# Optimization experiments

Measured on AMD Instinct MI355X. Metric: run time of the kernel, lower is better.

The kernel has to match this reference:

```python
import jax, jax.numpy as jnp
import numpy as np

B, S, H = 32, 1024, 768          # batch, seq_len, bert hidden
E, W, P = 128, 8, 512            # entities/sample, span width, rel pairs/sample
NT, NR = 5, 9                    # entity types, relation types
D1, HEADS1, D2, RD = 128, 2, 64, 32
REL_IN = 2 * D2 + RD + H         # 928


def _layernorm(x, g, b):
    m = x.mean(-1, keepdims=True)
    v = x.var(-1, keepdims=True)
    return (x - m) * jax.lax.rsqrt(v + 1e-5) * g + b


def _gat_dense(x, Wm, a_src, a_dst, bias, concat):
    # Fully-connected entity graph (incl. self-loops, PyG GATConv default).
    Bn, En, _ = x.shape
    Hh, D = a_src.shape
    h = (x @ Wm).reshape(Bn, En, Hh, D)                      # [B,E,h,D]
    s = jnp.einsum('behd,hd->beh', h, a_src)                 # source score
    d = jnp.einsum('behd,hd->beh', h, a_dst)                 # target score
    # edge j->i : e_ij = leaky_relu(s_j + d_i)
    e = jax.nn.leaky_relu(d[:, :, None, :] + s[:, None, :, :], 0.2)  # [B,i,j,h]
    alpha = jax.nn.softmax(e, axis=2)
    o = jnp.einsum('bijh,bjhd->bihd', alpha, h)
    o = o.reshape(Bn, En, Hh * D) if concat else o.mean(axis=2)
    return o + bias


def setup_inputs() -> dict:
    key = jax.random.key(0)
    ks = jax.random.split(key, 20)
    f = lambda k, shape: jax.random.normal(k, shape, jnp.float32) * 0.02
    return dict(
        sequence_output=jax.random.normal(ks[0], (B, S, H), jnp.float32),
        entity_starts=jax.random.randint(ks[1], (B, E), 0, S - W),
        entity_type_ids=jax.random.randint(ks[2], (B, E), 0, NT),
        pair_idx=jax.random.randint(ks[3], (B, P, 2), 0, E),
        rel_type_ids=jax.random.randint(ks[4], (B, P), 0, NR),
        entity_type_emb=f(ks[5], (NT, H)),
        rel_type_emb=f(ks[6], (NR, RD)),
        W1=f(ks[7], (H, HEADS1 * D1)), a_src1=f(ks[8], (HEADS1, D1)),
        a_dst1=f(ks[9], (HEADS1, D1)), b1=jnp.zeros((HEADS1 * D1,), jnp.float32),
        ln1_g=jnp.ones((HEADS1 * D1,), jnp.float32), ln1_b=jnp.zeros((HEADS1 * D1,), jnp.float32),
        W2=f(ks[10], (HEADS1 * D1, D2)), a_src2=f(ks[11], (1, D2)),
        a_dst2=f(ks[12], (1, D2)), b2=jnp.zeros((D2,), jnp.float32),
        ln2_g=jnp.ones((D2,), jnp.float32), ln2_b=jnp.zeros((D2,), jnp.float32),
        Wr1=f(ks[13], (REL_IN, 256)), br1=jnp.zeros((256,), jnp.float32),
        Wr2=f(ks[14], (256, 1)), br2=jnp.zeros((1,), jnp.float32),
    )


def reference(sequence_output, entity_starts, entity_type_ids, pair_idx, rel_type_ids,
              entity_type_emb, rel_type_emb,
              W1, a_src1, a_dst1, b1, ln1_g, ln1_b,
              W2, a_src2, a_dst2, b2, ln2_g, ln2_b,
              Wr1, br1, Wr2, br2):
    bidx = jnp.arange(B)[:, None]
    # --- per-entity attention pooling over span tokens ---
    tok_idx = entity_starts[:, :, None] + jnp.arange(W)            # [B,E,W]
    toks = sequence_output[jnp.arange(B)[:, None, None], tok_idx]  # [B,E,W,H]
    mean = toks.mean(axis=2)                                       # [B,E,H]
    attn = jax.nn.softmax(jnp.einsum('bewh,beh->bew', toks, mean), axis=-1)
    pooled = jnp.einsum('bew,bewh->beh', attn, toks)
    x = pooled + entity_type_emb[entity_type_ids]                  # [B,E,H]
    # --- 2-layer GAT over fully-connected entity graph ---
    x = jax.nn.elu(_layernorm(_gat_dense(x, W1, a_src1, a_dst1, b1, True), ln1_g, ln1_b))
    x = jax.nn.elu(_layernorm(_gat_dense(x, W2, a_src2, a_dst2, b2, False), ln2_g, ln2_b))
    # --- gather-concat relation MLP scoring ---
    cls = sequence_output[:, 0, :]                                 # [B,H]
    x1 = x[bidx, pair_idx[:, :, 0]]                                # [B,P,64]
    x2 = x[bidx, pair_idx[:, :, 1]]
    rel = rel_type_emb[rel_type_ids]                               # [B,P,32]
    pv = jnp.concatenate([x1, x2, rel, jnp.broadcast_to(cls[:, None, :], (B, P, H))], axis=-1)
    scores = (jax.nn.relu(pv @ Wr1 + br1) @ Wr2 + br2)[..., 0]     # [B,P]
    return scores
```

## Files before the change

kernel.cpp:

```cpp
#include <hip/hip_runtime.h>
#include <hip/hip_bf16.h>

#define BB 32
#define SS 1024
#define HHH 768
#define EE 128
#define WW 8
#define PP 512
#define RDD 32

typedef __attribute__((ext_vector_type(8))) short bf16x8;
typedef __attribute__((ext_vector_type(8))) unsigned short us8;
typedef __attribute__((ext_vector_type(4))) unsigned short us4;
typedef __attribute__((ext_vector_type(4))) float f32x4;

__device__ __forceinline__ unsigned short f2bf(float v) {
    __hip_bfloat16 h = __float2bfloat16(v);
    return *(unsigned short*)&h;
}

__global__ __launch_bounds__(256) void pool_prep_kernel(
    const float* __restrict__ seq, const int* __restrict__ starts,
    const int* __restrict__ types, const float* __restrict__ temb,
    unsigned short* __restrict__ xout,
    const float* __restrict__ W1, unsigned short* __restrict__ Wt,
    const float* __restrict__ Wr1, unsigned short* __restrict__ Wtr,
    const float* __restrict__ W2, unsigned short* __restrict__ W2t,
    const float* __restrict__ remb, unsigned short* __restrict__ rembb,
    float* __restrict__ basep) {
    int tid = threadIdx.x;
    __shared__ float sbuf[WW * HHH];
    __shared__ float scred[WW];
    __shared__ float attn_s[WW];

    if (blockIdx.x < BB * EE) {
        int be = blockIdx.x;
        int b = be >> 7;
        int start = starts[be];
        const float4* bp4 = (const float4*)(seq + ((size_t)b * SS + start) * HHH);
        for (int idx = tid; idx < WW * (HHH / 4); idx += 256) {
            int w = idx / (HHH / 4), h4 = idx % (HHH / 4);
            float4 v = bp4[(size_t)w * (HHH / 4) + h4];
            sbuf[w * HHH + h4 * 4 + 0] = v.x; sbuf[w * HHH + h4 * 4 + 1] = v.y;
            sbuf[w * HHH + h4 * 4 + 2] = v.z; sbuf[w * HHH + h4 * 4 + 3] = v.w;
        }
        __syncthreads();

        float sc[WW];
#pragma unroll
        for (int w = 0; w < WW; w++) sc[w] = 0.f;
#pragma unroll
        for (int c = 0; c < 3; c++) {
            int h = tid + 256 * c;
            float s = 0.f;
#pragma unroll
            for (int w = 0; w < WW; w++) s += sbuf[w * HHH + h];
            float m = s * (1.0f / WW);
#pragma unroll
            for (int w = 0; w < WW; w++) sc[w] += sbuf[w * HHH + h] * m;
        }
        if (tid < WW) scred[tid] = 0.f;
        __syncthreads();
        int lane = tid & 63;
#pragma unroll
        for (int w = 0; w < WW; w++) {
            float v = sc[w];
            for (int o = 32; o > 0; o >>= 1) v += __shfl_down(v, o, 64);
            if (lane == 0) atomicAdd(&scred[w], v);
        }
        __syncthreads();
        if (tid == 0) {
            float mx = scred[0];
            for (int w = 1; w < WW; w++) mx = fmaxf(mx, scred[w]);
            float ssum = 0.f;
            float a[WW];
            for (int w = 0; w < WW; w++) { a[w] = __expf(scred[w] - mx); ssum += a[w]; }
            float inv = 1.f / ssum;
            for (int w = 0; w < WW; w++) attn_s[w] = a[w] * inv;
        }
        __syncthreads();

        int t = types[be];
        const float* emb = temb + (size_t)t * HHH;
#pragma unroll
        for (int c = 0; c < 3; c++) {
            int h = tid + 256 * c;
            float p = 0.f;
#pragma unroll
            for (int w = 0; w < WW; w++) p += attn_s[w] * sbuf[w * HHH + h];
            xout[(size_t)be * HHH + h] = f2bf(p + emb[h]);
        }
        return;
    }

    int blk = blockIdx.x - BB * EE;
    if (blk < 48) {
        int k0 = blk * 16;
        for (int i = tid; i < 16 * 256; i += 256)
            sbuf[i] = W1[(size_t)(k0 + (i >> 8)) * 256 + (i & 255)];
        __syncthreads();
        int n = tid;
        us8 v0, v1;
#pragma unroll
        for (int kk = 0; kk < 8; kk++) v0[kk] = f2bf(sbuf[kk * 256 + n]);
#pragma unroll
        for (int kk = 0; kk < 8; kk++) v1[kk] = f2bf(sbuf[(8 + kk) * 256 + n]);
        *(us8*)(Wt + (size_t)n * HHH + k0) = v0;
        *(us8*)(Wt + (size_t)n * HHH + k0 + 8) = v1;
    } else if (blk < 58) {
        int k0 = (blk - 48) * 16;
        for (int i = tid; i < 16 * 256; i += 256)
            sbuf[i] = Wr1[(size_t)(k0 + (i >> 8)) * 256 + (i & 255)];
        __syncthreads();
        int n = tid;
        us8 v0, v1;
#pragma unroll
        for (int kk = 0; kk < 8; kk++) v0[kk] = f2bf(sbuf[kk * 256 + n]);
#pragma unroll
        for (int kk = 0; kk < 8; kk++) v1[kk] = f2bf(sbuf[(8 + kk) * 256 + n]);
        *(us8*)(Wtr + (size_t)n * 160 + k0) = v0;
        *(us8*)(Wtr + (size_t)n * 160 + k0 + 8) = v1;
    } else if (blk < 74) {
        int k0 = (blk - 58) * 16;
        for (int i = tid; i < 16 * 64; i += 256)
            sbuf[(i >> 6) * 64 + (i & 63)] = W2[(size_t)(k0 + (i >> 6)) * 64 + (i & 63)];
        __syncthreads();
        if (tid < 64) {
            int n = tid;
            us8 v0, v1;
#pragma unroll
            for (int kk = 0; kk < 8; kk++) v0[kk] = f2bf(sbuf[kk * 64 + n]);
#pragma unroll
            for (int kk = 0; kk < 8; kk++) v1[kk] = f2bf(sbuf[(8 + kk) * 64 + n]);
            *(us8*)(W2t + (size_t)n * 256 + k0) = v0;
            *(us8*)(W2t + (size_t)n * 256 + k0 + 8) = v1;
        }
    } else if (blk == 74) {
        for (int i = tid; i < 9 * RDD; i += 256) rembb[i] = f2bf(remb[i]);
    } else {
        int pc = blk - 75;
        int kc = pc % 12;
        int b = pc / 12;
        int n = tid;
        if (n < 64) sbuf[4096 + n] = seq[(size_t)b * SS * HHH + kc * 64 + n];
        __syncthreads();
        float acc = 0.f;
        const float* w = Wr1 + (size_t)(160 + kc * 64) * 256 + n;
#pragma unroll 16
        for (int k = 0; k < 64; k++) acc += sbuf[4096 + k] * w[(size_t)k * 256];
        basep[((size_t)kc * 32 + b) * 256 + n] = acc;
    }
}

__global__ __launch_bounds__(256) void gemm1_mfma_kernel(
    const unsigned short* __restrict__ Xb, const unsigned short* __restrict__ Wt,
    const float* __restrict__ asrc1, const float* __restrict__ adst1,
    unsigned short* __restrict__ h1Tg,
    float* __restrict__ ps_s, float* __restrict__ ps_d) {
    const int K = HHH;
    int n0 = blockIdx.x * 64;
    int m0 = blockIdx.y * 64;
    int tid = threadIdx.x;
    int wave = tid >> 6, lane = tid & 63;
    int wm = (wave >> 1) * 32, wn = (wave & 1) * 32;

    __shared__ __align__(16) unsigned short As[64][40];
    __shared__ __align__(16) unsigned short Bs[64][40];
    __shared__ __align__(16) unsigned short T[64][72];
    __shared__ float sdred[64][2][2];

    f32x4 acc[2][2] = {};
    int ar = tid >> 2;
    int ac = (tid & 3) * 8;
    int fr = lane & 15;
    int fk = (lane >> 4) * 8;

    for (int k0 = 0; k0 < K; k0 += 32) {
        us8 av = *(const us8*)(Xb + (size_t)(m0 + ar) * K + k0 + ac);
        us8 bv = *(const us8*)(Wt + (size_t)(n0 + ar) * K + k0 + ac);
        *(us8*)(&As[ar][ac]) = av;
        *(us8*)(&Bs[ar][ac]) = bv;
        __syncthreads();

        bf16x8 a0 = *(const bf16x8*)(&As[wm + fr][fk]);
        bf16x8 a1 = *(const bf16x8*)(&As[wm + 16 + fr][fk]);
        bf16x8 b0 = *(const bf16x8*)(&Bs[wn + fr][fk]);
        bf16x8 b1 = *(const bf16x8*)(&Bs[wn + 16 + fr][fk]);

        acc[0][0] = __builtin_amdgcn_mfma_f32_16x16x32_bf16(a0, b0, acc[0][0], 0, 0, 0);
        acc[0][1] = __builtin_amdgcn_mfma_f32_16x16x32_bf16(a0, b1, acc[0][1], 0, 0, 0);
        acc[1][0] = __builtin_amdgcn_mfma_f32_16x16x32_bf16(a1, b0, acc[1][0], 0, 0, 0);
        acc[1][1] = __builtin_amdgcn_mfma_f32_16x16x32_bf16(a1, b1, acc[1][1], 0, 0, 0);
        __syncthreads();
    }

    int crow = (lane >> 4) * 4;
    int ccol = lane & 15;
    int h = n0 >> 7;
    int nb = (n0 >> 6) & 1;
    int dbase = (n0 & 127) + wn;

    float asv[2], adv[2];
#pragma unroll
    for (int ni = 0; ni < 2; ni++) {
        int d = dbase + ni * 16 + ccol;
        asv[ni] = asrc1[h * 128 + d];
        adv[ni] = adst1[h * 128 + d];
    }

#pragma unroll
    for (int mi = 0; mi < 2; mi++) {
#pragma unroll
        for (int r = 0; r < 4; r++) {
            float sp = 0.f, dp = 0.f;
#pragma unroll
            for (int ni = 0; ni < 2; ni++) {
                float v = acc[mi][ni][r];
                T[wn + ni * 16 + ccol][wm + mi * 16 + crow + r] = f2bf(v);
                sp += v * asv[ni];
                dp += v * adv[ni];
            }
            for (int msk = 1; msk < 16; msk <<= 1) {
                sp += __shfl_xor(sp, msk, 64);
                dp += __shfl_xor(dp, msk, 64);
            }
            if ((lane & 15) == 0) {
                int row = wm + mi * 16 + crow + r;
                sdred[row][wn >> 5][0] = sp;
                sdred[row][wn >> 5][1] = dp;
            }
        }
    }
    __syncthreads();

    int b = m0 >> 7;
    int j0 = m0 & 127;
    if (tid < 64) {
        float spt = sdred[tid][0][0] + sdred[tid][1][0];
        float dpt = sdred[tid][0][1] + sdred[tid][1][1];
        size_t o = (size_t)nb * 8192 + ((size_t)(m0 + tid)) * 2 + h;
        ps_s[o] = spt;
        ps_d[o] = dpt;
    }
    {
        int d_l = tid >> 2, q = tid & 3;
        us8 v0 = *(const us8*)(&T[d_l][q * 16]);
        us8 v1 = *(const us8*)(&T[d_l][q * 16 + 8]);
        size_t go = ((size_t)(b * 2 + h) * 128 + (n0 & 127) + d_l) * 128 + j0 + q * 16;
        *(us8*)(h1Tg + go) = v0;
        *(us8*)(h1Tg + go + 8) = v1;
    }
}

__global__ __launch_bounds__(256) void gat1_gemm2_kernel(
    const unsigned short* __restrict__ h1Tg,
    const float* __restrict__ ps_s, const float* __restrict__ ps_d,
    const float* __restrict__ b1, const float* __restrict__ gamma,
    const float* __restrict__ beta,
    const unsigned short* __restrict__ W2t,
    const float* __restrict__ asrc2, const float* __restrict__ adst2,
    unsigned short* __restrict__ h2Tg, float* __restrict__ s2,
    float* __restrict__ d2) {
    int b = blockIdx.x >> 2;
    int c = blockIdx.x & 3;
    int tid = threadIdx.x;
    int wave = tid >> 6, lane = tid & 63;
    int h = wave >> 1, m = wave & 1;
    int fr = lane & 15;
    int fk = (lane >> 4) * 8;

    __shared__ __align__(16) unsigned short h1T[2][128][136];
    __shared__ float ssh[2][128];
    __shared__ float dsh[2][128];
    __shared__ float lnred[32][2][2];
    __shared__ __align__(16) unsigned short g1s[32][264];
    __shared__ float sdr2[32][2][2];
    __shared__ __align__(16) unsigned short t2[64][40];

    {
        const us8* src = (const us8*)(h1Tg + (size_t)b * 32768);
#pragma unroll
        for (int it = 0; it < 16; it++) {
            int i8 = tid + it * 256;
            int row = i8 >> 4;
            int j8 = i8 & 15;
            *(us8*)(&h1T[row >> 7][row & 127][j8 * 8]) = src[i8];
        }
        int hh = tid >> 7, j = tid & 127;
        size_t o = ((size_t)b * 128 + j) * 2 + hh;
        ssh[hh][j] = ps_s[o] + ps_s[o + 8192];
        dsh[hh][j] = ps_d[o] + ps_d[o + 8192];
    }
    __syncthreads();

    bf16x8 afrag[4];
    {
        float dd = dsh[h][c * 32 + m * 16 + fr];
        float ev[4][8];
        float mx = -1e30f;
#pragma unroll
        for (int ks = 0; ks < 4; ks++)
#pragma unroll
            for (int jj = 0; jj < 8; jj++) {
                float e = dd + ssh[h][ks * 32 + fk + jj];
                e = e >= 0.f ? e : 0.2f * e;
                ev[ks][jj] = e;
                mx = fmaxf(mx, e);
            }
        mx = fmaxf(mx, __shfl_xor(mx, 16, 64));
        mx = fmaxf(mx, __shfl_xor(mx, 32, 64));
        float sm = 0.f;
#pragma unroll
        for (int ks = 0; ks < 4; ks++)
#pragma unroll
            for (int jj = 0; jj < 8; jj++) {
                float e = __expf(ev[ks][jj] - mx);
                ev[ks][jj] = e;
                sm += e;
            }
        sm += __shfl_xor(sm, 16, 64);
        sm += __shfl_xor(sm, 32, 64);
        float inv = 1.f / sm;
#pragma unroll
        for (int ks = 0; ks < 4; ks++) {
            bf16x8 a;
#pragma unroll
            for (int jj = 0; jj < 8; jj++)
                a[jj] = (short)f2bf(ev[ks][jj] * inv);
            afrag[ks] = a;
        }
    }

    f32x4 acc[8] = {};
#pragma unroll
    for (int ks = 0; ks < 4; ks++)
#pragma unroll
        for (int ni = 0; ni < 8; ni++) {
            bf16x8 bv = *(const bf16x8*)(&h1T[h][ni * 16 + fr][ks * 32 + fk]);
            acc[ni] = __builtin_amdgcn_mfma_f32_16x16x32_bf16(
                afrag[ks], bv, acc[ni], 0, 0, 0);
        }

    int crow = (lane >> 4) * 4;
    int ccol = lane & 15;
    float bv_[8], gv[8], bev[8];
#pragma unroll
    for (int ni = 0; ni < 8; ni++) {
        int d = h * 128 + ni * 16 + ccol;
        bv_[ni] = b1[d]; gv[ni] = gamma[d]; bev[ni] = beta[d];
    }
    float vv[4][8];
#pragma unroll
    for (int r = 0; r < 4; r++) {
        float s = 0.f, q = 0.f;
#pragma unroll
        for (int ni = 0; ni < 8; ni++) {
            float v = acc[ni][r] + bv_[ni];
            vv[r][ni] = v;
            s += v;
            q += v * v;
        }
        s += __shfl_xor(s, 1, 64); s += __shfl_xor(s, 2, 64);
        s += __shfl_xor(s, 4, 64); s += __shfl_xor(s, 8, 64);
        q += __shfl_xor(q, 1, 64); q += __shfl_xor(q, 2, 64);
        q += __shfl_xor(q, 4, 64); q += __shfl_xor(q, 8, 64);
        if ((lane & 15) == 0) {
            lnred[m * 16 + crow + r][h][0] = s;
            lnred[m * 16 + crow + r][h][1] = q;
        }
    }
    __syncthreads();
#pragma unroll
    for (int r = 0; r < 4; r++) {
        int row = m * 16 + crow + r;
        float s = lnred[row][0][0] + lnred[row][1][0];
        float q = lnred[row][0][1] + lnred[row][1][1];
        float mean = s * (1.f / 256.f);
        float var = q * (1.f / 256.f) - mean * mean;
        float rs = rsqrtf(var + 1e-5f);
#pragma unroll
        for (int ni = 0; ni < 8; ni++) {
            float y = (vv[r][ni] - mean) * rs * gv[ni] + bev[ni];
            y = y > 0.f ? y : (__expf(y) - 1.f);
            g1s[row][h * 128 + ni * 16 + ccol] = f2bf(y);
        }
    }
    __syncthreads();

    int m2 = wave & 1;
    int nb = wave >> 1;
    f32x4 acc2[2] = {};
#pragma unroll
    for (int kc = 0; kc < 8; kc++) {
        bf16x8 a = *(const bf16x8*)(&g1s[m2 * 16 + fr][kc * 32 + fk]);
#pragma unroll
        for (int ni = 0; ni < 2; ni++) {
            bf16x8 wv = *(const bf16x8*)(W2t + (size_t)(nb * 32 + ni * 16 + fr) * 256 +
                                         kc * 32 + fk);
            acc2[ni] = __builtin_amdgcn_mfma_f32_16x16x32_bf16(a, wv, acc2[ni], 0, 0, 0);
        }
    }
    float as2[2], ad2[2];
#pragma unroll
    for (int ni = 0; ni < 2; ni++) {
        int n = nb * 32 + ni * 16 + ccol;
        as2[ni] = asrc2[n];
        ad2[ni] = adst2[n];
    }
#pragma unroll
    for (int r = 0; r < 4; r++) {
        int rl = m2 * 16 + crow + r;
        float sp = 0.f, dp = 0.f;
#pragma unroll
        for (int ni = 0; ni < 2; ni++) {
            float v = acc2[ni][r];
            t2[nb * 32 + ni * 16 + ccol][rl] = f2bf(v);
            sp += v * as2[ni];
            dp += v * ad2[ni];
        }
        for (int msk = 1; msk < 16; msk <<= 1) {
            sp += __shfl_xor(sp, msk, 64);
            dp += __shfl_xor(dp, msk, 64);
        }
        if ((lane & 15) == 0) {
            sdr2[rl][nb][0] = sp;
            sdr2[rl][nb][1] = dp;
        }
    }
    __syncthreads();
    if (tid < 32) {
        s2[(size_t)b * 128 + c * 32 + tid] = sdr2[tid][0][0] + sdr2[tid][1][0];
        d2[(size_t)b * 128 + c * 32 + tid] = sdr2[tid][0][1] + sdr2[tid][1][1];
    }
    {
        int d = tid >> 2, q = tid & 3;
        us8 v = *(const us8*)(&t2[d][q * 8]);
        *(us8*)(h2Tg + ((size_t)b * 64 + d) * 128 + c * 32 + q * 8) = v;
    }
}

__global__ __launch_bounds__(256) void gat2_fused_kernel(
    const unsigned short* __restrict__ h2Tg, const float* __restrict__ s2,
    const float* __restrict__ d2, const float* __restrict__ b2v,
    const float* __restrict__ gamma, const float* __restrict__ beta,
    unsigned short* __restrict__ x2b) {
    int b = blockIdx.x >> 1;
    int c = blockIdx.x & 1;
    int tid = threadIdx.x;
    int wave = tid >> 6, lane = tid & 63;
    int fr = lane & 15;
    int fk = (lane >> 4) * 8;

    __shared__ __align__(16) unsigned short h2T[64][136];
    __shared__ float ssh[128];
    __shared__ float dsh[128];

    {
        const us8* src = (const us8*)(h2Tg + (size_t)b * 64 * 128);
#pragma unroll
        for (int it = 0; it < 4; it++) {
            int i8 = tid + it * 256;
            int row = i8 >> 4;
            int j8 = i8 & 15;
            *(us8*)(&h2T[row][j8 * 8]) = src[i8];
        }
        if (tid < 128) ssh[tid] = s2[(size_t)b * 128 + tid];
        else dsh[tid - 128] = d2[(size_t)b * 128 + (tid - 128)];
    }
    __syncthreads();

    bf16x8 afrag[4];
    {
        float dd = dsh[c * 64 + wave * 16 + fr];
        float ev[4][8];
        float mx = -1e30f;
#pragma unroll
        for (int ks = 0; ks < 4; ks++)
#pragma unroll
            for (int jj = 0; jj < 8; jj++) {
                float e = dd + ssh[ks * 32 + fk + jj];
                e = e >= 0.f ? e : 0.2f * e;
                ev[ks][jj] = e;
                mx = fmaxf(mx, e);
            }
        mx = fmaxf(mx, __shfl_xor(mx, 16, 64));
        mx = fmaxf(mx, __shfl_xor(mx, 32, 64));
        float sm = 0.f;
#pragma unroll
        for (int ks = 0; ks < 4; ks++)
#pragma unroll
            for (int jj = 0; jj < 8; jj++) {
                float e = __expf(ev[ks][jj] - mx);
                ev[ks][jj] = e;
                sm += e;
            }
        sm += __shfl_xor(sm, 16, 64);
        sm += __shfl_xor(sm, 32, 64);
        float inv = 1.f / sm;
#pragma unroll
        for (int ks = 0; ks < 4; ks++) {
            bf16x8 a;
#pragma unroll
            for (int jj = 0; jj < 8; jj++)
                a[jj] = (short)f2bf(ev[ks][jj] * inv);
            afrag[ks] = a;
        }
    }

    f32x4 acc[4] = {};
#pragma unroll
    for (int ks = 0; ks < 4; ks++)
#pragma unroll
        for (int ni = 0; ni < 4; ni++) {
            bf16x8 bv = *(const bf16x8*)(&h2T[ni * 16 + fr][ks * 32 + fk]);
            acc[ni] = __builtin_amdgcn_mfma_f32_16x16x32_bf16(
                afrag[ks], bv, acc[ni], 0, 0, 0);
        }

    int crow = (lane >> 4) * 4;
    int ccol = lane & 15;
    float bv_[4], gv[4], bev[4];
#pragma unroll
    for (int ni = 0; ni < 4; ni++) {
        int d = ni * 16 + ccol;
        bv_[ni] = b2v[d]; gv[ni] = gamma[d]; bev[ni] = beta[d];
    }
#pragma unroll
    for (int r = 0; r < 4; r++) {
        float v[4];
        float s = 0.f;
#pragma unroll
        for (int ni = 0; ni < 4; ni++) {
            v[ni] = acc[ni][r] + bv_[ni];
            s += v[ni];
        }
        s += __shfl_xor(s, 1, 64); s += __shfl_xor(s, 2, 64);
        s += __shfl_xor(s, 4, 64); s += __shfl_xor(s, 8, 64);
        float mean = s * (1.f / 64.f);
        float sq = 0.f;
#pragma unroll
        for (int ni = 0; ni < 4; ni++) {
            float dv = v[ni] - mean;
            sq += dv * dv;
        }
        sq += __shfl_xor(sq, 1, 64); sq += __shfl_xor(sq, 2, 64);
        sq += __shfl_xor(sq, 4, 64); sq += __shfl_xor(sq, 8, 64);
        float rs = rsqrtf(sq * (1.f / 64.f) + 1e-5f);
        int i = c * 64 + wave * 16 + crow + r;
        unsigned short* dst = x2b + (size_t)(b * 128 + i) * 64;
#pragma unroll
        for (int ni = 0; ni < 4; ni++) {
            float y = (v[ni] - mean) * rs * gv[ni] + bev[ni];
            y = y > 0.f ? y : (__expf(y) - 1.f);
            dst[ni * 16 + ccol] = f2bf(y);
        }
    }
}

__global__ __launch_bounds__(256) void score_mfma_kernel(
    const unsigned short* __restrict__ x2b, const float* __restrict__ basep,
    const float* __restrict__ br1,
    const int* __restrict__ pair_idx, const int* __restrict__ rel_ids,
    const unsigned short* __restrict__ rembb, const unsigned short* __restrict__ Wtr,
    const float* __restrict__ Wr2, const float* __restrict__ br2,
    float* __restrict__ out) {
    int blk = blockIdx.x;
    int b = blk >> 3;
    int p0 = (blk & 7) * 64;
    int tid = threadIdx.x;
    int wave = tid >> 6, lane = tid & 63;
    int wn = wave * 64;

    __shared__ __align__(16) unsigned short As[64][168];
    __shared__ __align__(16) unsigned short Bs[256][40];
    __shared__ float sred[64][4];
    __shared__ int prs[64][3];

    if (tid < 64) {
        int p = p0 + tid;
        prs[tid][0] = pair_idx[((size_t)b * PP + p) * 2 + 0];
        prs[tid][1] = pair_idx[((size_t)b * PP + p) * 2 + 1];
        prs[tid][2] = rel_ids[(size_t)b * PP + p];
    }
    __syncthreads();
    for (int it = 0; it < 10; it++) {
        int idx = tid + it * 256;
        int m = idx / 40, c = idx % 40;
        int k0 = c * 4;
        us4 v;
        if (k0 < 64)
            v = *(const us4*)(x2b + ((size_t)b * EE + prs[m][0]) * 64 + k0);
        else if (k0 < 128)
            v = *(const us4*)(x2b + ((size_t)b * EE + prs[m][1]) * 64 + (k0 - 64));
        else
            v = *(const us4*)(rembb + prs[m][2] * RDD + (k0 - 128));
        *(us4*)(&As[m][k0]) = v;
    }

    f32x4 acc[4][4] = {};
    int fr = lane & 15;
    int fk = (lane >> 4) * 8;

    for (int kc = 0; kc < 5; kc++) {
        for (int it = 0; it < 4; it++) {
            int i = tid + it * 256;
            int n = i >> 2, c = i & 3;
            *(us8*)(&Bs[n][c * 8]) =
                *(const us8*)(Wtr + (size_t)n * 160 + kc * 32 + c * 8);
        }
        __syncthreads();
        bf16x8 a[4], bv[4];
#pragma unroll
        for (int mi = 0; mi < 4; mi++)
            a[mi] = *(const bf16x8*)(&As[mi * 16 + fr][kc * 32 + fk]);
#pragma unroll
        for (int ni = 0; ni < 4; ni++)
            bv[ni] = *(const bf16x8*)(&Bs[wn + ni * 16 + fr][fk]);
#pragma unroll
        for (int mi = 0; mi < 4; mi++)
#pragma unroll
            for (int ni = 0; ni < 4; ni++)
                acc[mi][ni] = __builtin_amdgcn_mfma_f32_16x16x32_bf16(
                    a[mi], bv[ni], acc[mi][ni], 0, 0, 0);
        __syncthreads();
    }

    int crow = (lane >> 4) * 4;
    int ccol = lane & 15;
    float basev[4], w2v[4];
#pragma unroll
    for (int ni = 0; ni < 4; ni++) {
        int n = wn + ni * 16 + ccol;
        float bb = br1[n];
#pragma unroll
        for (int kc = 0; kc < 12; kc++)
            bb += basep[((size_t)kc * 32 + b) * 256 + n];
        basev[ni] = bb;
        w2v[ni] = Wr2[n];
    }
#pragma unroll
    for (int mi = 0; mi < 4; mi++) {
#pragma unroll
        for (int r = 0; r < 4; r++) {
            float p = 0.f;
#pragma unroll
            for (int ni = 0; ni < 4; ni++)
                p += fmaxf(acc[mi][ni][r] + basev[ni], 0.f) * w2v[ni];
            for (int msk = 1; msk < 16; msk <<= 1)
                p += __shfl_xor(p, msk, 64);
            if ((lane & 15) == 0)
                sred[mi * 16 + crow + r][wave] = p;
        }
    }
    __syncthreads();
    if (tid < 64) {
        float s = sred[tid][0] + sred[tid][1] + sred[tid][2] + sred[tid][3] + br2[0];
        out[(size_t)b * PP + p0 + tid] = s;
    }
}

extern "C" void kernel_launch(void* const* d_in, const int* in_sizes, int n_in,
                              void* d_out, int out_size, void* d_ws, size_t ws_size,
                              hipStream_t stream) {
    (void)in_sizes; (void)n_in; (void)out_size; (void)ws_size;
    const float* seq      = (const float*)d_in[0];
    const int*   starts   = (const int*)d_in[1];
    const int*   types    = (const int*)d_in[2];
    const int*   pair_idx = (const int*)d_in[3];
    const int*   rel_ids  = (const int*)d_in[4];
    const float* temb     = (const float*)d_in[5];
    const float* remb     = (const float*)d_in[6];
    const float* W1       = (const float*)d_in[7];
    const float* a_src1   = (const float*)d_in[8];
    const float* a_dst1   = (const float*)d_in[9];
    const float* b1       = (const float*)d_in[10];
    const float* ln1_g    = (const float*)d_in[11];
    const float* ln1_b    = (const float*)d_in[12];
    const float* W2       = (const float*)d_in[13];
    const float* a_src2   = (const float*)d_in[14];
    const float* a_dst2   = (const float*)d_in[15];
    const float* b2       = (const float*)d_in[16];
    const float* ln2_g    = (const float*)d_in[17];
    const float* ln2_b    = (const float*)d_in[18];
    const float* Wr1      = (const float*)d_in[19];
    const float* br1      = (const float*)d_in[20];
    const float* Wr2      = (const float*)d_in[21];
    const float* br2      = (const float*)d_in[22];
    float* out = (float*)d_out;

    unsigned short* xb    = (unsigned short*)d_ws;
    unsigned short* Wt    = xb + (size_t)4096 * 768;
    unsigned short* Wtr   = Wt + (size_t)256 * 768;
    unsigned short* W2t   = Wtr + (size_t)256 * 160;
    unsigned short* rembb = W2t + (size_t)64 * 256;
    unsigned short* h1Tg  = rembb + 512;
    unsigned short* h2Tg  = h1Tg + (size_t)4096 * 256;
    unsigned short* x2b   = h2Tg + (size_t)32 * 64 * 128;
    float* fbase = (float*)(x2b + (size_t)4096 * 64);
    float* ps_s  = fbase;
    float* ps_d  = ps_s + 2 * 8192;
    float* s2    = ps_d + 2 * 8192;
    float* d2    = s2 + 4096;
    float* basep = d2 + 4096;

    pool_prep_kernel<<<BB * EE + 75 + 12 * 32, 256, 0, stream>>>(
        seq, starts, types, temb, xb, W1, Wt, Wr1, Wtr, W2, W2t, remb, rembb, basep);
    gemm1_mfma_kernel<<<dim3(4, 64), 256, 0, stream>>>(xb, Wt, a_src1, a_dst1,
                                                       h1Tg, ps_s, ps_d);
    gat1_gemm2_kernel<<<BB * 4, 256, 0, stream>>>(h1Tg, ps_s, ps_d, b1, ln1_g, ln1_b,
                                                  W2t, a_src2, a_dst2, h2Tg, s2, d2);
    gat2_fused_kernel<<<BB * 2, 256, 0, stream>>>(h2Tg, s2, d2, b2, ln2_g, ln2_b, x2b);
    score_mfma_kernel<<<BB * PP / 64, 256, 0, stream>>>(x2b, basep, br1, pair_idx,
                                                        rel_ids, rembb, Wtr, Wr2,
                                                        br2, out);
}
```

Before: 228.9 us.

## Fuse GAT layer-2 into relation scoring kernel, recomputing per pair block

Merges the second GAT layer (attention softmax, aggregation MFMA, layernorm, ELU) into the relation-scoring kernel. Each of the 8 pair-blocks per batch recomputes the full 128-entity layer-2 output into shared memory and gathers pair features from LDS instead of a global x2b buffer. Shared memory is reused through a union. This removes one kernel launch and the global round trip of x2b, at the cost of doing the GAT2 work 8 times per batch (redundant compute, though small).

Measured after the change: 229.3 us. About the same (+0.1%).

```diff
diff --git a/kernel.cpp b/kernel.cpp
--- a/kernel.cpp
+++ b/kernel.cpp
@@ -439,127 +439,26 @@
     }
 }
 
-__global__ __launch_bounds__(256) void gat2_fused_kernel(
+struct K45G {
+    unsigned short h2T[64][136];
+    float ssh[128];
+    float dsh[128];
+};
+struct K45S {
+    unsigned short As[64][168];
+    unsigned short Bs[256][40];
+    float sred[64][4];
+};
+union K45U {
+    K45G g;
+    K45S s;
+};
+
+__global__ __launch_bounds__(256) void gat2_score_kernel(
     const unsigned short* __restrict__ h2Tg, const float* __restrict__ s2,
     const float* __restrict__ d2, const float* __restrict__ b2v,
     const float* __restrict__ gamma, const float* __restrict__ beta,
-    unsigned short* __restrict__ x2b) {
-    int b = blockIdx.x >> 1;
-    int c = blockIdx.x & 1;
-    int tid = threadIdx.x;
-    int wave = tid >> 6, lane = tid & 63;
-    int fr = lane & 15;
-    int fk = (lane >> 4) * 8;
-
-    __shared__ __align__(16) unsigned short h2T[64][136];
-    __shared__ float ssh[128];
-    __shared__ float dsh[128];
-
-    {
-        const us8* src = (const us8*)(h2Tg + (size_t)b * 64 * 128);
-#pragma unroll
-        for (int it = 0; it < 4; it++) {
-            int i8 = tid + it * 256;
-            int row = i8 >> 4;
-            int j8 = i8 & 15;
-            *(us8*)(&h2T[row][j8 * 8]) = src[i8];
-        }
-        if (tid < 128) ssh[tid] = s2[(size_t)b * 128 + tid];
-        else dsh[tid - 128] = d2[(size_t)b * 128 + (tid - 128)];
-    }
-    __syncthreads();
-
-    bf16x8 afrag[4];
-    {
-        float dd = dsh[c * 64 + wave * 16 + fr];
-        float ev[4][8];
-        float mx = -1e30f;
-#pragma unroll
-        for (int ks = 0; ks < 4; ks++)
-#pragma unroll
-            for (int jj = 0; jj < 8; jj++) {
-                float e = dd + ssh[ks * 32 + fk + jj];
-                e = e >= 0.f ? e : 0.2f * e;
-                ev[ks][jj] = e;
-                mx = fmaxf(mx, e);
-            }
-        mx = fmaxf(mx, __shfl_xor(mx, 16, 64));
-        mx = fmaxf(mx, __shfl_xor(mx, 32, 64));
-        float sm = 0.f;
-#pragma unroll
-        for (int ks = 0; ks < 4; ks++)
-#pragma unroll
-            for (int jj = 0; jj < 8; jj++) {
-                float e = __expf(ev[ks][jj] - mx);
-                ev[ks][jj] = e;
-                sm += e;
-            }
-        sm += __shfl_xor(sm, 16, 64);
-        sm += __shfl_xor(sm, 32, 64);
-        float inv = 1.f / sm;
-#pragma unroll
-        for (int ks = 0; ks < 4; ks++) {
-            bf16x8 a;
-#pragma unroll
-            for (int jj = 0; jj < 8; jj++)
-                a[jj] = (short)f2bf(ev[ks][jj] * inv);
-            afrag[ks] = a;
-        }
-    }
-
-    f32x4 acc[4] = {};
-#pragma unroll
-    for (int ks = 0; ks < 4; ks++)
-#pragma unroll
-        for (int ni = 0; ni < 4; ni++) {
-            bf16x8 bv = *(const bf16x8*)(&h2T[ni * 16 + fr][ks * 32 + fk]);
-            acc[ni] = __builtin_amdgcn_mfma_f32_16x16x32_bf16(
-                afrag[ks], bv, acc[ni], 0, 0, 0);
-        }
-
-    int crow = (lane >> 4) * 4;
-    int ccol = lane & 15;
-    float bv_[4], gv[4], bev[4];
-#pragma unroll
-    for (int ni = 0; ni < 4; ni++) {
-        int d = ni * 16 + ccol;
-        bv_[ni] = b2v[d]; gv[ni] = gamma[d]; bev[ni] = beta[d];
-    }
-#pragma unroll
-    for (int r = 0; r < 4; r++) {
-        float v[4];
-        float s = 0.f;
-#pragma unroll
-        for (int ni = 0; ni < 4; ni++) {
-            v[ni] = acc[ni][r] + bv_[ni];
-            s += v[ni];
-        }
-        s += __shfl_xor(s, 1, 64); s += __shfl_xor(s, 2, 64);
-        s += __shfl_xor(s, 4, 64); s += __shfl_xor(s, 8, 64);
-        float mean = s * (1.f / 64.f);
-        float sq = 0.f;
-#pragma unroll
-        for (int ni = 0; ni < 4; ni++) {
-            float dv = v[ni] - mean;
-            sq += dv * dv;
-        }
-        sq += __shfl_xor(sq, 1, 64); sq += __shfl_xor(sq, 2, 64);
-        sq += __shfl_xor(sq, 4, 64); sq += __shfl_xor(sq, 8, 64);
-        float rs = rsqrtf(sq * (1.f / 64.f) + 1e-5f);
-        int i = c * 64 + wave * 16 + crow + r;
-        unsigned short* dst = x2b + (size_t)(b * 128 + i) * 64;
-#pragma unroll
-        for (int ni = 0; ni < 4; ni++) {
-            float y = (v[ni] - mean) * rs * gv[ni] + bev[ni];
-            y = y > 0.f ? y : (__expf(y) - 1.f);
-            dst[ni * 16 + ccol] = f2bf(y);
-        }
-    }
-}
-
-__global__ __launch_bounds__(256) void score_mfma_kernel(
-    const unsigned short* __restrict__ x2b, const float* __restrict__ basep,
-    const float* __restrict__ br1,
+    const float* __restrict__ basep, const float* __restrict__ br1,
     const int* __restrict__ pair_idx, const int* __restrict__ rel_ids,
     const unsigned short* __restrict__ rembb, const unsigned short* __restrict__ Wtr,
     const float* __restrict__ Wr2, const float* __restrict__ br2,
@@ -569,53 +468,154 @@
     int p0 = (blk & 7) * 64;
     int tid = threadIdx.x;
     int wave = tid >> 6, lane = tid & 63;
-    int wn = wave * 64;
-
-    __shared__ __align__(16) unsigned short As[64][168];
-    __shared__ __align__(16) unsigned short Bs[256][40];
-    __shared__ float sred[64][4];
+    int fr = lane & 15;
+    int fk = (lane >> 4) * 8;
+    int crow = (lane >> 4) * 4;
+    int ccol = lane & 15;
+
+    __shared__ __align__(16) K45U u;
+    __shared__ __align__(16) unsigned short x2s[128][68];
     __shared__ int prs[64][3];
 
-    if (tid < 64) {
-        int p = p0 + tid;
-        prs[tid][0] = pair_idx[((size_t)b * PP + p) * 2 + 0];
-        prs[tid][1] = pair_idx[((size_t)b * PP + p) * 2 + 1];
-        prs[tid][2] = rel_ids[(size_t)b * PP + p];
+    {
+        const us8* src = (const us8*)(h2Tg + (size_t)b * 64 * 128);
+#pragma unroll
+        for (int it = 0; it < 4; it++) {
+            int i8 = tid + it * 256;
+            int row = i8 >> 4;
+            int j8 = i8 & 15;
+            *(us8*)(&u.g.h2T[row][j8 * 8]) = src[i8];
+        }
+        if (tid < 128) u.g.ssh[tid] = s2[(size_t)b * 128 + tid];
+        else u.g.dsh[tid - 128] = d2[(size_t)b * 128 + (tid - 128)];
+        if (tid < 64) {
+            int pp = p0 + tid;
+            prs[tid][0] = pair_idx[((size_t)b * PP + pp) * 2 + 0];
+            prs[tid][1] = pair_idx[((size_t)b * PP + pp) * 2 + 1];
+            prs[tid][2] = rel_ids[(size_t)b * PP + pp];
+        }
     }
     __syncthreads();
+
+#pragma unroll
+    for (int c2 = 0; c2 < 2; c2++) {
+        bf16x8 afrag[4];
+        {
+            float dd = u.g.dsh[c2 * 64 + wave * 16 + fr];
+            float ev[4][8];
+            float mx = -1e30f;
+#pragma unroll
+            for (int ks = 0; ks < 4; ks++)
+#pragma unroll
+                for (int jj = 0; jj < 8; jj++) {
+                    float e = dd + u.g.ssh[ks * 32 + fk + jj];
+                    e = e >= 0.f ? e : 0.2f * e;
+                    ev[ks][jj] = e;
+                    mx = fmaxf(mx, e);
+                }
+            mx = fmaxf(mx, __shfl_xor(mx, 16, 64));
+            mx = fmaxf(mx, __shfl_xor(mx, 32, 64));
+            float sm = 0.f;
+#pragma unroll
+            for (int ks = 0; ks < 4; ks++)
+#pragma unroll
+                for (int jj = 0; jj < 8; jj++) {
+                    float e = __expf(ev[ks][jj] - mx);
+                    ev[ks][jj] = e;
+                    sm += e;
+                }
+            sm += __shfl_xor(sm, 16, 64);
+            sm += __shfl_xor(sm, 32, 64);
+            float inv = 1.f / sm;
+#pragma unroll
+            for (int ks = 0; ks < 4; ks++) {
+                bf16x8 a;
+#pragma unroll
+                for (int jj = 0; jj < 8; jj++)
+                    a[jj] = (short)f2bf(ev[ks][jj] * inv);
+                afrag[ks] = a;
+            }
+        }
+
+        f32x4 acc[4] = {};
+#pragma unroll
+        for (int ks = 0; ks < 4; ks++)
+#pragma unroll
+            for (int ni = 0; ni < 4; ni++) {
+                bf16x8 bv = *(const bf16x8*)(&u.g.h2T[ni * 16 + fr][ks * 32 + fk]);
+                acc[ni] = __builtin_amdgcn_mfma_f32_16x16x32_bf16(
+                    afrag[ks], bv, acc[ni], 0, 0, 0);
+            }
+
+        float bv_[4], gv[4], bev[4];
+#pragma unroll
+        for (int ni = 0; ni < 4; ni++) {
+            int d = ni * 16 + ccol;
+            bv_[ni] = b2v[d]; gv[ni] = gamma[d]; bev[ni] = beta[d];
+        }
+#pragma unroll
+        for (int r = 0; r < 4; r++) {
+            float v[4];
+            float s = 0.f;
+#pragma unroll
+            for (int ni = 0; ni < 4; ni++) {
+                v[ni] = acc[ni][r] + bv_[ni];
+                s += v[ni];
+            }
+            s += __shfl_xor(s, 1, 64); s += __shfl_xor(s, 2, 64);
+            s += __shfl_xor(s, 4, 64); s += __shfl_xor(s, 8, 64);
+            float mean = s * (1.f / 64.f);
+            float sq = 0.f;
+#pragma unroll
+            for (int ni = 0; ni < 4; ni++) {
+                float dv = v[ni] - mean;
+                sq += dv * dv;
+            }
+            sq += __shfl_xor(sq, 1, 64); sq += __shfl_xor(sq, 2, 64);
+            sq += __shfl_xor(sq, 4, 64); sq += __shfl_xor(sq, 8, 64);
+            float rs = rsqrtf(sq * (1.f / 64.f) + 1e-5f);
+            int i = c2 * 64 + wave * 16 + crow + r;
+#pragma unroll
+            for (int ni = 0; ni < 4; ni++) {
+                float y = (v[ni] - mean) * rs * gv[ni] + bev[ni];
+                y = y > 0.f ? y : (__expf(y) - 1.f);
+                x2s[i][ni * 16 + ccol] = f2bf(y);
+            }
+        }
+    }
+    __syncthreads();
+
     for (int it = 0; it < 10; it++) {
         int idx = tid + it * 256;
         int m = idx / 40, c = idx % 40;
         int k0 = c * 4;
         us4 v;
         if (k0 < 64)
-            v = *(const us4*)(x2b + ((size_t)b * EE + prs[m][0]) * 64 + k0);
+            v = *(const us4*)(&x2s[prs[m][0]][k0]);
         else if (k0 < 128)
-            v = *(const us4*)(x2b + ((size_t)b * EE + prs[m][1]) * 64 + (k0 - 64));
+            v = *(const us4*)(&x2s[prs[m][1]][k0 - 64]);
         else
             v = *(const us4*)(rembb + prs[m][2] * RDD + (k0 - 128));
-        *(us4*)(&As[m][k0]) = v;
+        *(us4*)(&u.s.As[m][k0]) = v;
     }
 
     f32x4 acc[4][4] = {};
-    int fr = lane & 15;
-    int fk = (lane >> 4) * 8;
-
+    int wn = wave * 64;
     for (int kc = 0; kc < 5; kc++) {
         for (int it = 0; it < 4; it++) {
             int i = tid + it * 256;
             int n = i >> 2, c = i & 3;
-            *(us8*)(&Bs[n][c * 8]) =
+            *(us8*)(&u.s.Bs[n][c * 8]) =
                 *(const us8*)(Wtr + (size_t)n * 160 + kc * 32 + c * 8);
         }
         __syncthreads();
         bf16x8 a[4], bv[4];
 #pragma unroll
         for (int mi = 0; mi < 4; mi++)
-            a[mi] = *(const bf16x8*)(&As[mi * 16 + fr][kc * 32 + fk]);
+            a[mi] = *(const bf16x8*)(&u.s.As[mi * 16 + fr][kc * 32 + fk]);
 #pragma unroll
         for (int ni = 0; ni < 4; ni++)
-            bv[ni] = *(const bf16x8*)(&Bs[wn + ni * 16 + fr][fk]);
+            bv[ni] = *(const bf16x8*)(&u.s.Bs[wn + ni * 16 + fr][fk]);
 #pragma unroll
         for (int mi = 0; mi < 4; mi++)
 #pragma unroll
@@ -625,8 +625,6 @@
         __syncthreads();
     }
 
-    int crow = (lane >> 4) * 4;
-    int ccol = lane & 15;
     float basev[4], w2v[4];
 #pragma unroll
     for (int ni = 0; ni < 4; ni++) {
@@ -649,12 +647,13 @@
             for (int msk = 1; msk < 16; msk <<= 1)
                 p += __shfl_xor(p, msk, 64);
             if ((lane & 15) == 0)
-                sred[mi * 16 + crow + r][wave] = p;
+                u.s.sred[mi * 16 + crow + r][wave] = p;
         }
     }
     __syncthreads();
     if (tid < 64) {
-        float s = sred[tid][0] + sred[tid][1] + sred[tid][2] + sred[tid][3] + br2[0];
+        float s = u.s.sred[tid][0] + u.s.sred[tid][1] + u.s.sred[tid][2] +
+                  u.s.sred[tid][3] + br2[0];
         out[(size_t)b * PP + p0 + tid] = s;
     }
 }
@@ -695,8 +694,7 @@
     unsigned short* rembb = W2t + (size_t)64 * 256;
     unsigned short* h1Tg  = rembb + 512;
     unsigned short* h2Tg  = h1Tg + (size_t)4096 * 256;
-    unsigned short* x2b   = h2Tg + (size_t)32 * 64 * 128;
-    float* fbase = (float*)(x2b + (size_t)4096 * 64);
+    float* fbase = (float*)(h2Tg + (size_t)32 * 64 * 128);
     float* ps_s  = fbase;
     float* ps_d  = ps_s + 2 * 8192;
     float* s2    = ps_d + 2 * 8192;
@@ -704,13 +702,13 @@
     float* basep = d2 + 4096;
 
     pool_prep_kernel<<<BB * EE + 75 + 12 * 32, 256, 0, stream>>>(
-        seq, starts, types, temb, xb, W1, Wt, Wr1, Wtr, W2, W2t, remb, rembb, basep);
+        seq, starts, types, temb, xb, W1, Wt, Wr1, Wtr, W2, W2t, remb, rembb,
+        basep);
     gemm1_mfma_kernel<<<dim3(4, 64), 256, 0, stream>>>(xb, Wt, a_src1, a_dst1,
                                                        h1Tg, ps_s, ps_d);
     gat1_gemm2_kernel<<<BB * 4, 256, 0, stream>>>(h1Tg, ps_s, ps_d, b1, ln1_g, ln1_b,
                                                   W2t, a_src2, a_dst2, h2Tg, s2, d2);
-    gat2_fused_kernel<<<BB * 2, 256, 0, stream>>>(h2Tg, s2, d2, b2, ln2_g, ln2_b, x2b);
-    score_mfma_kernel<<<BB * PP / 64, 256, 0, stream>>>(x2b, basep, br1, pair_idx,
-                                                        rel_ids, rembb, Wtr, Wr2,
-                                                        br2, out);
+    gat2_score_kernel<<<BB * PP / 64, 256, 0, stream>>>(
+        h2Tg, s2, d2, b2, ln2_g, ln2_b, basep, br1, pair_idx, rel_ids,
+        rembb, Wtr, Wr2, br2, out);
 }
```
